# Kernel tuning notes

Measured on AMD Instinct MI355X. Metric: run time of the kernel, lower is better.

The kernel has to match this reference:

```python
import jax, jax.numpy as jnp
import numpy as np

DILATIONS_REST = (2, 4, 8, 16, 32, 64)


def _causal_conv(x, v, g, b, dilation):
    # weight-norm: w = g * v / ||v||_(in,k) per out-channel
    norm = jnp.sqrt(jnp.sum(v * v, axis=(1, 2), keepdims=True))
    w = g[:, None, None] * v / norm                      # [O, I, K]
    pad = (v.shape[2] - 1) * dilation                    # left-only causal pad
    y = jax.lax.conv_general_dilated(
        x, w, window_strides=(1,), padding=[(pad, 0)],
        rhs_dilation=(dilation,), dimension_numbers=('NCH', 'OIH', 'NCH'))
    return y + b[None, :, None]


def setup_inputs() -> dict:
    key = jax.random.key(0)
    ks = jax.random.split(key, 16)
    B, T, V, E = 64, 2048, 32000, 300
    inp = {
        'inputs': jax.random.randint(ks[0], (B, T), 0, V),
        'de_feature': jax.random.normal(ks[1], (B, 11), dtype=jnp.float32),
        'emb': jax.random.normal(ks[2], (V, E), dtype=jnp.float32) * 0.02,
        'v0': jax.random.normal(ks[3], (128, 300, 5), dtype=jnp.float32) * 0.05,
        'g0': jnp.ones((128,), dtype=jnp.float32),
        'b0': jax.random.normal(ks[4], (128,), dtype=jnp.float32) * 0.01,
        'vr': jax.random.normal(ks[5], (6, 128, 128, 5), dtype=jnp.float32) * 0.05,
        'gr': jnp.ones((6, 128), dtype=jnp.float32),
        'br': jax.random.normal(ks[6], (6, 128), dtype=jnp.float32) * 0.01,
        'fc1_w': jax.random.normal(ks[7], (64, 139), dtype=jnp.float32) * 0.08,
        'fc1_b': jnp.zeros((64,), dtype=jnp.float32),
        'fc2_w': jax.random.normal(ks[8], (32, 64), dtype=jnp.float32) * 0.12,
        'fc2_b': jnp.zeros((32,), dtype=jnp.float32),
        'fc3_w': jax.random.normal(ks[9], (1, 32), dtype=jnp.float32) * 0.17,
        'fc3_b': jnp.zeros((1,), dtype=jnp.float32),
    }
    return inp


def reference(inputs, de_feature, emb, v0, g0, b0, vr, gr, br,
              fc1_w, fc1_b, fc2_w, fc2_b, fc3_w, fc3_b):
    x = emb[inputs]                       # [B, T, 300]
    x = jnp.transpose(x, (0, 2, 1))       # [B, 300, T]
    x = jax.nn.relu(_causal_conv(x, v0, g0, b0, 1))
    for i, d in enumerate(DILATIONS_REST):
        x = jax.nn.relu(_causal_conv(x, vr[i], gr[i], br[i], d))
    emb_v = x[:, :, -1]                   # last timestep [B, 128]
    combo = jnp.concatenate([emb_v, de_feature], axis=1)  # [B, 139]
    h = jax.nn.relu(combo @ fc1_w.T + fc1_b)
    h = jax.nn.relu(h @ fc2_w.T + fc2_b)
    logits = h @ fc3_w.T + fc3_b          # [B, 1]
    return logits
```

## Files before the change

### kernel.cpp

```cpp
#include <hip/hip_runtime.h>


typedef __attribute__((ext_vector_type(8))) short bfrag8;
typedef __attribute__((ext_vector_type(4))) float floatx4;
typedef __attribute__((ext_vector_type(4))) short short4v;
typedef __attribute__((ext_vector_type(4))) float float4v;

__device__ __forceinline__ unsigned short f2bf(float f) {
  union { float f; unsigned u; } v; v.f = f;
  unsigned r = v.u + 0x7fffu + ((v.u >> 16) & 1u);
  return (unsigned short)(r >> 16);
}
__device__ __forceinline__ float bf2f(unsigned short h) {
  union { unsigned u; float f; } v; v.u = ((unsigned)h) << 16;
  return v.f;
}
__device__ __forceinline__ int swz(int row) { return ((row >> 1) & 7) << 4; }

__global__ __launch_bounds__(512)
void k_wnorm(const float* __restrict__ v0, const float* __restrict__ g0,
             const float* __restrict__ vr, const float* __restrict__ gr,
             unsigned short* __restrict__ WB0, unsigned short* __restrict__ WBr) {
  const int gw = (blockIdx.x << 3) + (threadIdx.x >> 6);
  const int lane = threadIdx.x & 63;
  if (gw < 128) {
    const int o = gw;
    const float* v = v0 + o * 1500;
    float ss = 0.f;
    for (int i = lane; i < 1500; i += 64) { const float x = v[i]; ss += x * x; }
#pragma unroll
    for (int off = 32; off; off >>= 1) ss += __shfl_xor(ss, off, 64);
    const float scale = g0[o] * rsqrtf(ss);
    const int ot = o >> 4;
    for (int kk = lane; kk < 1600; kk += 64) {
      const int tap = kk / 320, c = kk % 320;
      const float w = (c < 300) ? v[c * 5 + tap] * scale : 0.f;
      const int ks = kk >> 5;
      const int li = (o & 15) | (((kk >> 3) & 3) << 4);
      WB0[(((ot * 50 + ks) * 64 + li) << 3) | (kk & 7)] = f2bf(w);
    }
  } else {
    const int idx = gw - 128;
    const int l = idx >> 7, o = idx & 127;
    const float* v = vr + (size_t)(l * 128 + o) * 640;
    float ss = 0.f;
#pragma unroll
    for (int i = 0; i < 10; ++i) { const float x = v[lane + (i << 6)]; ss += x * x; }
#pragma unroll
    for (int off = 32; off; off >>= 1) ss += __shfl_xor(ss, off, 64);
    const float scale = gr[l * 128 + o] * rsqrtf(ss);
    unsigned short* WB = WBr + (size_t)l * 81920;
    const int ot = o >> 4;
#pragma unroll
    for (int i = 0; i < 10; ++i) {
      const int kk = lane + (i << 6);
      const int tap = kk >> 7, c = kk & 127;
      const float w = v[c * 5 + tap] * scale;
      const int ks = kk >> 5;
      const int li = (o & 15) | (((kk >> 3) & 3) << 4);
      WB[(((ot * 20 + ks) * 64 + li) << 3) | (kk & 7)] = f2bf(w);
    }
  }
}

template<int NMT>
__device__ __forceinline__ void l0_part(const char* embBuf, char* a0buf,
    const unsigned short* __restrict__ WB0, const float* __restrict__ b0,
    int mt0, int og, int qb, int kg, int lane) {
  floatx4 acc[NMT][2];
#pragma unroll
  for (int m = 0; m < NMT; ++m) {
    acc[m][0] = floatx4{0.f, 0.f, 0.f, 0.f};
    acc[m][1] = floatx4{0.f, 0.f, 0.f, 0.f};
  }
  const unsigned short* wb0 = WB0 + (size_t)((((og << 1) * 50) << 6) + lane) * 8;
#pragma unroll
  for (int tap = 0; tap < 5; ++tap) {
    bfrag8 bf0[10], bf1[10];
#pragma unroll
    for (int cs = 0; cs < 10; ++cs) {
      const int ks = tap * 10 + cs;
      bf0[cs] = *(const bfrag8*)(wb0 + (ks << 9));
      bf1[cs] = *(const bfrag8*)(wb0 + ((ks + 50) << 9));
    }
#pragma unroll
    for (int cs = 0; cs < 10; ++cs) {
      const int cb = (cs << 6) + (kg << 4);
#pragma unroll
      for (int m = 0; m < NMT; ++m) {
        const int row = (((mt0 + m) << 4) + qb) * 2 + tap;
        const bfrag8 a = *(const bfrag8*)(embBuf + row * 656 + cb);
        acc[m][0] = __builtin_amdgcn_mfma_f32_16x16x32_bf16(a, bf0[cs], acc[m][0], 0, 0, 0);
        acc[m][1] = __builtin_amdgcn_mfma_f32_16x16x32_bf16(a, bf1[cs], acc[m][1], 0, 0, 0);
      }
    }
  }
  const int o0 = (og << 5) + qb;
  const float bv0 = b0[o0], bv1 = b0[o0 + 16];
#pragma unroll
  for (int m = 0; m < NMT; ++m)
#pragma unroll
    for (int r = 0; r < 4; ++r) {
      const int qq = ((mt0 + m) << 4) + (kg << 2) + r;
      *(unsigned short*)(a0buf + (((qq << 8) + (o0 << 1)) ^ swz(qq))) =
          f2bf(fmaxf(acc[m][0][r] + bv0, 0.f));
      *(unsigned short*)(a0buf + (((qq << 8) + ((o0 + 16) << 1)) ^ swz(qq))) =
          f2bf(fmaxf(acc[m][1][r] + bv1, 0.f));
    }
}

template<int NMTW, int NOTW, int MCAP>
__device__ __forceinline__ void conv_l(const char* bi, char* bo,
    const unsigned short* __restrict__ WBl, const float* __restrict__ bias,
    int mt0, int og, int qb, int kg, int lane) {
  floatx4 acc[NMTW][NOTW];
#pragma unroll
  for (int m = 0; m < NMTW; ++m)
#pragma unroll
    for (int j = 0; j < NOTW; ++j) acc[m][j] = floatx4{0.f, 0.f, 0.f, 0.f};
#pragma unroll
  for (int tap = 0; tap < 5; ++tap) {
    bfrag8 bfs[NOTW][4];
#pragma unroll
    for (int j = 0; j < NOTW; ++j)
#pragma unroll
      for (int cs = 0; cs < 4; ++cs)
        bfs[j][cs] = *(const bfrag8*)(WBl +
            (size_t)((((og * NOTW + j) * 20 + (tap << 2) + cs) << 6) + lane) * 8);
#pragma unroll
    for (int cs = 0; cs < 4; ++cs) {
      const int cb = (cs << 6) + (kg << 4);
#pragma unroll
      for (int m = 0; m < NMTW; ++m) {
        const int row = (((mt0 + m) << 4) + qb) * 2 + tap;
        const bfrag8 a = *(const bfrag8*)(bi + (((row << 8) + cb) ^ swz(row)));
#pragma unroll
        for (int j = 0; j < NOTW; ++j)
          acc[m][j] = __builtin_amdgcn_mfma_f32_16x16x32_bf16(a, bfs[j][cs], acc[m][j], 0, 0, 0);
      }
    }
  }
#pragma unroll
  for (int m = 0; m < NMTW; ++m)
#pragma unroll
    for (int j = 0; j < NOTW; ++j) {
      const int o = ((og * NOTW + j) << 4) + qb;
      const float bv = bias[o];
#pragma unroll
      for (int r = 0; r < 4; ++r) {
        const int qq = ((mt0 + m) << 4) + (kg << 2) + r;
        if (qq < MCAP)
          *(unsigned short*)(bo + (((qq << 8) + (o << 1)) ^ swz(qq))) =
              f2bf(fmaxf(acc[m][j][r] + bv, 0.f));
      }
    }
}

__global__ __launch_bounds__(512, 1)
void k_conv(const int* __restrict__ tokens, const float* __restrict__ emb,
            const unsigned short* __restrict__ WB0, const unsigned short* __restrict__ WBr,
            const float* __restrict__ b0, const float* __restrict__ br,
            unsigned short* __restrict__ L2out) {
  __shared__ char lds[143008];
  char* embBuf = lds;
  char* a0buf  = lds + 107584;
  char* l1buf  = lds + 133184;
  int*  toks   = (int*)(lds + 142400);
  const int tid = threadIdx.x;
  const int qt = blockIdx.x, b = blockIdx.y;
  if (tid < 152) {
    const int p = (qt << 7) + tid;
    toks[tid] = (tid < 149 && p < 509) ? tokens[(b << 11) + 1539 + p] : -1;
  }
  __syncthreads();
  for (int idx = tid; idx < 151 * 80; idx += 512) {
    const int r = idx / 80, s = idx - r * 80;
    short4v o = {0, 0, 0, 0};
    const int tok = toks[r];
    if (tok >= 0 && s < 75) {
      const float4v v = *(const float4v*)(emb + (size_t)tok * 300 + (s << 2));
      o[0] = (short)f2bf(v[0]); o[1] = (short)f2bf(v[1]);
      o[2] = (short)f2bf(v[2]); o[3] = (short)f2bf(v[3]);
    }
    *(short4v*)(embBuf + r * 656 + (s << 3)) = o;
  }
  __syncthreads();
  const int lane = tid & 63, w = tid >> 6;
  const int og = w & 3, mgh = w >> 2;
  const int qb = lane & 15, kg = lane >> 4;

  if (mgh == 0) l0_part<3>(embBuf, a0buf, WB0, b0, 0, og, qb, kg, lane);
  else          l0_part<2>(embBuf, a0buf, WB0, b0, 3, og, qb, kg, lane);
  __syncthreads();
  if (mgh == 0) conv_l<2, 2, 36>(a0buf, l1buf, WBr, br, 0, og, qb, kg, lane);
  else          conv_l<1, 2, 36>(a0buf, l1buf, WBr, br, 2, og, qb, kg, lane);
  __syncthreads();
  {
    floatx4 acc = {0.f, 0.f, 0.f, 0.f};
    const unsigned short* wbl = WBr + 81920;
#pragma unroll
    for (int tap = 0; tap < 5; ++tap) {
      bfrag8 bfs[4];
#pragma unroll
      for (int cs = 0; cs < 4; ++cs)
        bfs[cs] = *(const bfrag8*)(wbl +
            (size_t)(((w * 20 + (tap << 2) + cs) << 6) + lane) * 8);
#pragma unroll
      for (int cs = 0; cs < 4; ++cs) {
        const int cb = (cs << 6) + (kg << 4);
        const int row = (qb << 1) + tap;
        const bfrag8 a = *(const bfrag8*)(l1buf + (((row << 8) + cb) ^ swz(row)));
        acc = __builtin_amdgcn_mfma_f32_16x16x32_bf16(a, bfs[cs], acc, 0, 0, 0);
      }
    }
    const int o = (w << 4) + qb;
    const float bv = br[128 + o];
    unsigned short* ob = L2out + ((size_t)b << 13);
#pragma unroll
    for (int r = 0; r < 4; ++r) {
      const int q2 = (qt << 4) + (kg << 2) + r;
      if (q2 < 61) ob[(q2 << 7) + o] = f2bf(fmaxf(acc[r] + bv, 0.f));
    }
  }
}

__global__ __launch_bounds__(512, 1)
void k_tail3(const unsigned short* __restrict__ L2out, const unsigned short* __restrict__ WBr,
             const float* __restrict__ br, const float* __restrict__ de,
             const float* __restrict__ w1, const float* __restrict__ b1,
             const float* __restrict__ w2, const float* __restrict__ b2,
             const float* __restrict__ w3, const float* __restrict__ b3,
             float* __restrict__ out) {
  __shared__ char lds2[68 * 256 + 36 * 256 + 384];
  char* bufS = lds2;
  char* bufT = lds2 + 68 * 256;
  float* h1 = (float*)(lds2 + 68 * 256 + 36 * 256);
  float* h2 = h1 + 64;
  const int tid = threadIdx.x, b = blockIdx.x;
  const int lane = tid & 63, w = tid >> 6;
  const int qb = lane & 15, kg = lane >> 4;

  const char* l2b = (const char*)(L2out + ((size_t)b << 13));
  for (int idx = tid; idx < 61 * 16; idx += 512) {
    const int r = idx >> 4, s = idx & 15;
    *(float4v*)(bufS + (((r << 8) + (s << 4)) ^ swz(r))) =
        *(const float4v*)(l2b + (r << 8) + (s << 4));
  }
  __syncthreads();

  conv_l<1, 2, 32>(bufS, bufT, WBr + 2 * 81920, br + 256, w & 1, w >> 1, qb, kg, lane);
  __syncthreads();
  conv_l<1, 1, 16>(bufT, bufS, WBr + 3 * 81920, br + 384, 0, w, qb, kg, lane);
  __syncthreads();
  conv_l<1, 1, 16>(bufS, bufT, WBr + 4 * 81920, br + 512, 0, w, qb, kg, lane);
  __syncthreads();
  conv_l<1, 1, 16>(bufT, bufS, WBr + 5 * 81920, br + 640, 0, w, qb, kg, lane);
  __syncthreads();

  const unsigned short* o6 = (const unsigned short*)bufS;
  {
    const int o1 = tid >> 3, part = tid & 7;
    const int j0 = part * 18;
    const int j1 = (j0 + 18 < 139) ? j0 + 18 : 139;
    float s = 0.f;
    const float* wrow = w1 + o1 * 139;
    for (int j = j0; j < j1; ++j) {
      const float x = (j < 128) ? bf2f(o6[j]) : de[b * 11 + (j - 128)];
      s += wrow[j] * x;
    }
    s += __shfl_down(s, 4, 64);
    s += __shfl_down(s, 2, 64);
    s += __shfl_down(s, 1, 64);
    if (part == 0) h1[o1] = fmaxf(s + b1[o1], 0.f);
  }
  __syncthreads();
  if (tid < 64) {
    const int o2 = tid >> 1, part = tid & 1;
    float s = 0.f;
    const float* wrow = w2 + o2 * 64 + part * 32;
    for (int j = 0; j < 32; ++j) s += wrow[j] * h1[part * 32 + j];
    s += __shfl_down(s, 1, 64);
    if (part == 0) h2[o2] = fmaxf(s + b2[o2], 0.f);
  }
  __syncthreads();
  if (tid < 32) {
    float s = w3[tid] * h2[tid];
    s += __shfl_down(s, 16, 64);
    s += __shfl_down(s, 8, 64);
    s += __shfl_down(s, 4, 64);
    s += __shfl_down(s, 2, 64);
    s += __shfl_down(s, 1, 64);
    if (tid == 0) out[b] = s + b3[0];
  }
}

extern "C" void kernel_launch(void* const* d_in, const int* in_sizes, int n_in,
                              void* d_out, int out_size, void* d_ws, size_t ws_size,
                              hipStream_t stream) {
  const int*   tokens = (const int*)  d_in[0];
  const float* de     = (const float*)d_in[1];
  const float* emb    = (const float*)d_in[2];
  const float* v0     = (const float*)d_in[3];
  const float* g0     = (const float*)d_in[4];
  const float* b0     = (const float*)d_in[5];
  const float* vr     = (const float*)d_in[6];
  const float* gr     = (const float*)d_in[7];
  const float* br     = (const float*)d_in[8];
  const float* w1     = (const float*)d_in[9];
  const float* b1     = (const float*)d_in[10];
  const float* w2     = (const float*)d_in[11];
  const float* b2     = (const float*)d_in[12];
  const float* w3     = (const float*)d_in[13];
  const float* b3     = (const float*)d_in[14];
  float* out = (float*)d_out;

  char* w = (char*)d_ws;
  unsigned short* WB0   = (unsigned short*)(w + 0);
  unsigned short* WBr   = (unsigned short*)(w + 409600);
  unsigned short* L2out = (unsigned short*)(w + 1392640);

  hipLaunchKernelGGL(k_wnorm, dim3(112), dim3(512), 0, stream, v0, g0, vr, gr, WB0, WBr);
  hipLaunchKernelGGL(k_conv, dim3(4, 64), dim3(512), 0, stream,
                     tokens, emb, WB0, WBr, b0, br, L2out);
  hipLaunchKernelGGL(k_tail3, dim3(64), dim3(512), 0, stream,
                     L2out, WBr, br, de, w1, b1, w2, b2, w3, b3, out);
}
```

Before: 69.68 us.

## Split fused conv kernel into separate layer-0 and layers-1/2 kernels via global buffer

Layer 0 of the dilated conv stack moves out of the fused k_conv kernel into its own k_conv0g kernel. That kernel uses a small LDS footprint, twice the blocks and launch bounds allowing four blocks per CU, and writes bf16 activations to a global A0 buffer. A new k_conv12 kernel stages those activations back into LDS and runs layers 1 and 2. The aim is to cut the roughly 143 KB LDS requirement that limited occupancy to one block per CU and to spread the heavy layer-0 GEMM over more waves. The cost is an extra kernel launch and a global round trip for the intermediate activations.

```diff
diff --git a/kernel.cpp b/kernel.cpp
--- a/kernel.cpp
+++ b/kernel.cpp
@@ -63,117 +63,20 @@
   }
 }
 
-template<int NMT>
-__device__ __forceinline__ void l0_part(const char* embBuf, char* a0buf,
-    const unsigned short* __restrict__ WB0, const float* __restrict__ b0,
-    int mt0, int og, int qb, int kg, int lane) {
-  floatx4 acc[NMT][2];
-#pragma unroll
-  for (int m = 0; m < NMT; ++m) {
-    acc[m][0] = floatx4{0.f, 0.f, 0.f, 0.f};
-    acc[m][1] = floatx4{0.f, 0.f, 0.f, 0.f};
-  }
-  const unsigned short* wb0 = WB0 + (size_t)((((og << 1) * 50) << 6) + lane) * 8;
-#pragma unroll
-  for (int tap = 0; tap < 5; ++tap) {
-    bfrag8 bf0[10], bf1[10];
-#pragma unroll
-    for (int cs = 0; cs < 10; ++cs) {
-      const int ks = tap * 10 + cs;
-      bf0[cs] = *(const bfrag8*)(wb0 + (ks << 9));
-      bf1[cs] = *(const bfrag8*)(wb0 + ((ks + 50) << 9));
-    }
-#pragma unroll
-    for (int cs = 0; cs < 10; ++cs) {
-      const int cb = (cs << 6) + (kg << 4);
-#pragma unroll
-      for (int m = 0; m < NMT; ++m) {
-        const int row = (((mt0 + m) << 4) + qb) * 2 + tap;
-        const bfrag8 a = *(const bfrag8*)(embBuf + row * 656 + cb);
-        acc[m][0] = __builtin_amdgcn_mfma_f32_16x16x32_bf16(a, bf0[cs], acc[m][0], 0, 0, 0);
-        acc[m][1] = __builtin_amdgcn_mfma_f32_16x16x32_bf16(a, bf1[cs], acc[m][1], 0, 0, 0);
-      }
-    }
-  }
-  const int o0 = (og << 5) + qb;
-  const float bv0 = b0[o0], bv1 = b0[o0 + 16];
-#pragma unroll
-  for (int m = 0; m < NMT; ++m)
-#pragma unroll
-    for (int r = 0; r < 4; ++r) {
-      const int qq = ((mt0 + m) << 4) + (kg << 2) + r;
-      *(unsigned short*)(a0buf + (((qq << 8) + (o0 << 1)) ^ swz(qq))) =
-          f2bf(fmaxf(acc[m][0][r] + bv0, 0.f));
-      *(unsigned short*)(a0buf + (((qq << 8) + ((o0 + 16) << 1)) ^ swz(qq))) =
-          f2bf(fmaxf(acc[m][1][r] + bv1, 0.f));
-    }
-}
-
-template<int NMTW, int NOTW, int MCAP>
-__device__ __forceinline__ void conv_l(const char* bi, char* bo,
-    const unsigned short* __restrict__ WBl, const float* __restrict__ bias,
-    int mt0, int og, int qb, int kg, int lane) {
-  floatx4 acc[NMTW][NOTW];
-#pragma unroll
-  for (int m = 0; m < NMTW; ++m)
-#pragma unroll
-    for (int j = 0; j < NOTW; ++j) acc[m][j] = floatx4{0.f, 0.f, 0.f, 0.f};
-#pragma unroll
-  for (int tap = 0; tap < 5; ++tap) {
-    bfrag8 bfs[NOTW][4];
-#pragma unroll
-    for (int j = 0; j < NOTW; ++j)
-#pragma unroll
-      for (int cs = 0; cs < 4; ++cs)
-        bfs[j][cs] = *(const bfrag8*)(WBl +
-            (size_t)((((og * NOTW + j) * 20 + (tap << 2) + cs) << 6) + lane) * 8);
-#pragma unroll
-    for (int cs = 0; cs < 4; ++cs) {
-      const int cb = (cs << 6) + (kg << 4);
-#pragma unroll
-      for (int m = 0; m < NMTW; ++m) {
-        const int row = (((mt0 + m) << 4) + qb) * 2 + tap;
-        const bfrag8 a = *(const bfrag8*)(bi + (((row << 8) + cb) ^ swz(row)));
-#pragma unroll
-        for (int j = 0; j < NOTW; ++j)
-          acc[m][j] = __builtin_amdgcn_mfma_f32_16x16x32_bf16(a, bfs[j][cs], acc[m][j], 0, 0, 0);
-      }
-    }
-  }
-#pragma unroll
-  for (int m = 0; m < NMTW; ++m)
-#pragma unroll
-    for (int j = 0; j < NOTW; ++j) {
-      const int o = ((og * NOTW + j) << 4) + qb;
-      const float bv = bias[o];
-#pragma unroll
-      for (int r = 0; r < 4; ++r) {
-        const int qq = ((mt0 + m) << 4) + (kg << 2) + r;
-        if (qq < MCAP)
-          *(unsigned short*)(bo + (((qq << 8) + (o << 1)) ^ swz(qq))) =
-              f2bf(fmaxf(acc[m][j][r] + bv, 0.f));
-      }
-    }
-}
-
-__global__ __launch_bounds__(512, 1)
-void k_conv(const int* __restrict__ tokens, const float* __restrict__ emb,
-            const unsigned short* __restrict__ WB0, const unsigned short* __restrict__ WBr,
-            const float* __restrict__ b0, const float* __restrict__ br,
-            unsigned short* __restrict__ L2out) {
-  __shared__ char lds[143008];
-  char* embBuf = lds;
-  char* a0buf  = lds + 107584;
-  char* l1buf  = lds + 133184;
-  int*  toks   = (int*)(lds + 142400);
+__global__ __launch_bounds__(512, 4)
+void k_conv0g(const int* __restrict__ tokens, const float* __restrict__ emb,
+              const unsigned short* __restrict__ WB0, const float* __restrict__ b0,
+              unsigned short* __restrict__ A0) {
+  __shared__ char embBuf[67 * 656];
+  __shared__ int toks[68];
   const int tid = threadIdx.x;
   const int qt = blockIdx.x, b = blockIdx.y;
-  if (tid < 152) {
-    const int p = (qt << 7) + tid;
-    toks[tid] = (tid < 149 && p < 509) ? tokens[(b << 11) + 1539 + p] : -1;
-  }
-  __syncthreads();
-  for (int idx = tid; idx < 151 * 80; idx += 512) {
+  if (tid < 68) {
+    const int p = (qt << 6) + tid;
+    toks[tid] = (tid < 67 && p < 509) ? tokens[(b << 11) + 1539 + p] : -1;
+  }
+  __syncthreads();
+  for (int idx = tid; idx < 67 * 80; idx += 512) {
     const int r = idx / 80, s = idx - r * 80;
     short4v o = {0, 0, 0, 0};
     const int tok = toks[r];
@@ -186,14 +89,111 @@
   }
   __syncthreads();
   const int lane = tid & 63, w = tid >> 6;
+  const int qb = lane & 15, kg = lane >> 4;
+  floatx4 acc[2];
+  acc[0] = floatx4{0.f, 0.f, 0.f, 0.f};
+  acc[1] = floatx4{0.f, 0.f, 0.f, 0.f};
+  const unsigned short* wb0 = WB0 + (size_t)(((w * 50) << 6) + lane) * 8;
+#pragma unroll
+  for (int tap = 0; tap < 5; ++tap) {
+    bfrag8 bf[10];
+#pragma unroll
+    for (int cs = 0; cs < 10; ++cs)
+      bf[cs] = *(const bfrag8*)(wb0 + ((tap * 10 + cs) << 9));
+#pragma unroll
+    for (int cs = 0; cs < 10; ++cs) {
+      const int cb = (cs << 6) + (kg << 4);
+#pragma unroll
+      for (int m = 0; m < 2; ++m) {
+        const int row = (((m << 4) + qb) << 1) + tap;
+        const bfrag8 a = *(const bfrag8*)(embBuf + row * 656 + cb);
+        acc[m] = __builtin_amdgcn_mfma_f32_16x16x32_bf16(a, bf[cs], acc[m], 0, 0, 0);
+      }
+    }
+  }
+  unsigned short* ob = A0 + (((size_t)b << 8) + (qt << 5)) * 128;
+  const int o = (w << 4) + qb;
+  const float bv = b0[o];
+#pragma unroll
+  for (int m = 0; m < 2; ++m)
+#pragma unroll
+    for (int r = 0; r < 4; ++r) {
+      const int ql = (m << 4) + (kg << 2) + r;
+      ob[ql * 128 + o] = f2bf(fmaxf(acc[m][r] + bv, 0.f));
+    }
+}
+
+template<int NMTW, int NOTW, int MCAP>
+__device__ __forceinline__ void conv_l(const char* bi, char* bo,
+    const unsigned short* __restrict__ WBl, const float* __restrict__ bias,
+    int mt0, int og, int qb, int kg, int lane) {
+  floatx4 acc[NMTW][NOTW];
+#pragma unroll
+  for (int m = 0; m < NMTW; ++m)
+#pragma unroll
+    for (int j = 0; j < NOTW; ++j) acc[m][j] = floatx4{0.f, 0.f, 0.f, 0.f};
+#pragma unroll
+  for (int tap = 0; tap < 5; ++tap) {
+    bfrag8 bfs[NOTW][4];
+#pragma unroll
+    for (int j = 0; j < NOTW; ++j)
+#pragma unroll
+      for (int cs = 0; cs < 4; ++cs)
+        bfs[j][cs] = *(const bfrag8*)(WBl +
+            (size_t)((((og * NOTW + j) * 20 + (tap << 2) + cs) << 6) + lane) * 8);
+#pragma unroll
+    for (int cs = 0; cs < 4; ++cs) {
+      const int cb = (cs << 6) + (kg << 4);
+#pragma unroll
+      for (int m = 0; m < NMTW; ++m) {
+        const int row = (((mt0 + m) << 4) + qb) * 2 + tap;
+        const bfrag8 a = *(const bfrag8*)(bi + (((row << 8) + cb) ^ swz(row)));
+#pragma unroll
+        for (int j = 0; j < NOTW; ++j)
+          acc[m][j] = __builtin_amdgcn_mfma_f32_16x16x32_bf16(a, bfs[j][cs], acc[m][j], 0, 0, 0);
+      }
+    }
+  }
+#pragma unroll
+  for (int m = 0; m < NMTW; ++m)
+#pragma unroll
+    for (int j = 0; j < NOTW; ++j) {
+      const int o = ((og * NOTW + j) << 4) + qb;
+      const float bv = bias[o];
+#pragma unroll
+      for (int r = 0; r < 4; ++r) {
+        const int qq = ((mt0 + m) << 4) + (kg << 2) + r;
+        if (qq < MCAP)
+          *(unsigned short*)(bo + (((qq << 8) + (o << 1)) ^ swz(qq))) =
+              f2bf(fmaxf(acc[m][j][r] + bv, 0.f));
+      }
+    }
+}
+
+__global__ __launch_bounds__(512, 1)
+void k_conv12(const unsigned short* __restrict__ A0,
+              const unsigned short* __restrict__ WBr, const float* __restrict__ br,
+              unsigned short* __restrict__ L2out) {
+  __shared__ char a0stage[100 * 256];
+  __shared__ char l1buf[36 * 256];
+  const int tid = threadIdx.x;
+  const int qt = blockIdx.x, b = blockIdx.y;
+  const char* a0b = (const char*)(A0 + ((size_t)b << 15));
+  for (int idx = tid; idx < 100 * 16; idx += 512) {
+    const int r = idx >> 4, s = idx & 15;
+    float4v v = {0.f, 0.f, 0.f, 0.f};
+    if (r < 73) {
+      int rs = (qt << 6) + r; if (rs > 255) rs = 255;
+      v = *(const float4v*)(a0b + (rs << 8) + (s << 4));
+    }
+    *(float4v*)(a0stage + (((r << 8) + (s << 4)) ^ swz(r))) = v;
+  }
+  __syncthreads();
+  const int lane = tid & 63, w = tid >> 6;
   const int og = w & 3, mgh = w >> 2;
   const int qb = lane & 15, kg = lane >> 4;
-
-  if (mgh == 0) l0_part<3>(embBuf, a0buf, WB0, b0, 0, og, qb, kg, lane);
-  else          l0_part<2>(embBuf, a0buf, WB0, b0, 3, og, qb, kg, lane);
-  __syncthreads();
-  if (mgh == 0) conv_l<2, 2, 36>(a0buf, l1buf, WBr, br, 0, og, qb, kg, lane);
-  else          conv_l<1, 2, 36>(a0buf, l1buf, WBr, br, 2, og, qb, kg, lane);
+  if (mgh == 0) conv_l<2, 2, 36>(a0stage, l1buf, WBr, br, 0, og, qb, kg, lane);
+  else          conv_l<1, 2, 36>(a0stage, l1buf, WBr, br, 2, og, qb, kg, lane);
   __syncthreads();
   {
     floatx4 acc = {0.f, 0.f, 0.f, 0.f};
@@ -317,11 +317,13 @@
   char* w = (char*)d_ws;
   unsigned short* WB0   = (unsigned short*)(w + 0);
   unsigned short* WBr   = (unsigned short*)(w + 409600);
-  unsigned short* L2out = (unsigned short*)(w + 1392640);
+  unsigned short* A0    = (unsigned short*)(w + 1392640);
+  unsigned short* L2out = (unsigned short*)(w + 5586944);
 
   hipLaunchKernelGGL(k_wnorm, dim3(112), dim3(512), 0, stream, v0, g0, vr, gr, WB0, WBr);
-  hipLaunchKernelGGL(k_conv, dim3(4, 64), dim3(512), 0, stream,
-                     tokens, emb, WB0, WBr, b0, br, L2out);
+  hipLaunchKernelGGL(k_conv0g, dim3(8, 64), dim3(512), 0, stream,
+                     tokens, emb, WB0, b0, A0);
+  hipLaunchKernelGGL(k_conv12, dim3(4, 64), dim3(512), 0, stream, A0, WBr, br, L2out);
   hipLaunchKernelGGL(k_tail3, dim3(64), dim3(512), 0, stream,
                      L2out, WBr, br, de, w1, b1, w2, b2, w3, b3, out);
 }
```

Result: faster. 65.83 us, median of 3 (-5.5%).
